# Kernel optimization log

Measured on AMD Instinct MI355X. Metric: run time of the kernel, lower is better.

Reference implementation:

```python
import jax, jax.numpy as jnp
import numpy as np

S = 1024   # query_len == key_len (self-attention)
B = 4      # batch
E = 1024   # embed_dim
H = 16     # num_heads
D = E // H # head_dim = 64
PE = 2 * S # positional table rows


def setup_inputs() -> dict:
    rng = jax.random.key(0)
    ks = jax.random.split(rng, 12)
    f = lambda k, sh, s: jax.random.normal(k, sh, dtype=jnp.float32) * s
    W = 0.02  # weight scale (xavier-ish for E=1024)
    return {
        'query': f(ks[0], (S, B, E), 1.0),
        'key': f(ks[1], (S, B, E), 1.0),
        'value': f(ks[2], (S, B, E), 1.0),
        'pe': f(ks[3], (PE, E), 1.0),
        'w_q': f(ks[4], (E, E), W),
        'w_k': f(ks[5], (E, E), W),
        'w_v': f(ks[6], (E, E), W),
        'w_k_pos': f(ks[7], (E, E), W),
        'content_bias': f(ks[8], (H, D), 0.02),
        'pos_bias': f(ks[9], (H, D), 0.02),
        'w_out': f(ks[10], (E, E), W),
        'b_out': f(ks[11], (E,), 0.02),
    }


def _rel_shift(pos):
    # pos: [B, H, Q, M] with M = 2*K - 1. Transformer-XL pad/narrow shift trick.
    Bn, h, Q, M = pos.shape
    p = jnp.pad(pos, ((0, 0), (0, 0), (0, 1), (0, 1)))          # [B,H,Q+1,M+1]
    p = p.reshape(Bn, h, (Q + 1) * (M + 1))
    p = p[:, :, M // 2: M // 2 + M * Q].reshape(Bn, h, Q, M)
    return p[..., :(M + 1) // 2]                                 # [B,H,Q,K]


def reference(query, key, value, pe, w_q, w_k, w_v, w_k_pos,
              content_bias, pos_bias, w_out, b_out):
    Q, Bn, Em = query.shape
    K = key.shape[0]
    h, d = content_bias.shape
    scaling = d ** -0.5

    # projections (nn.Linear: x @ W.T), split heads -> [B,H,len,d]
    q = (query @ w_q.T).reshape(Q, Bn, h, d).transpose(1, 2, 0, 3)
    k = (key   @ w_k.T).reshape(K, Bn, h, d).transpose(1, 2, 0, 3)
    v = (value @ w_v.T).reshape(K, Bn, h, d).transpose(1, 2, 0, 3)

    # relative position keys: centered slice of pe table, size 2K-1
    M = 2 * K - 1
    lower = pe.shape[0] // 2 - K + 1  # offset = 0
    k_pos = (pe[lower:lower + M] @ w_k_pos.T).reshape(M, h, d).transpose(1, 0, 2)  # [H,M,d]

    content = jnp.einsum('bhqd,bhkd->bhqk', q + content_bias[None, :, None, :], k)
    pos = jnp.einsum('bhqd,hmd->bhqm', q + pos_bias[None, :, None, :], k_pos)
    pos = _rel_shift(pos)  # [B,H,Q,K]

    attn = jax.nn.softmax((content + pos) * scaling, axis=-1)
    out = jnp.einsum('bhqk,bhkd->bhqd', attn, v)        # [B,H,Q,d]
    out = out.transpose(2, 0, 1, 3).reshape(Q, Bn, Em)  # [Q,B,E]
    return out @ w_out.T + b_out
```

## Files before the change

### kernel.cpp

```cpp
#include <hip/hip_runtime.h>


typedef short s16x8 __attribute__((ext_vector_type(8)));
typedef __bf16 bf16x8 __attribute__((ext_vector_type(8)));
typedef float f32x4 __attribute__((ext_vector_type(4)));
typedef unsigned int u32;

__device__ __forceinline__ float b2f(short s) {
  u32 u = ((u32)(unsigned short)s) << 16;
  return __builtin_bit_cast(float, u);
}
__device__ __forceinline__ short f2b(float f) {
  u32 u = __builtin_bit_cast(u32, f);
  u32 r = u + 0x7FFFu + ((u >> 16) & 1u);
  return (short)(r >> 16);
}

__device__ __forceinline__ f32x4 mfma_bf16(s16x8 a, s16x8 b, f32x4 c) {
  return __builtin_amdgcn_mfma_f32_16x16x32_bf16(
      __builtin_bit_cast(bf16x8, a), __builtin_bit_cast(bf16x8, b), c, 0, 0, 0);
}

__device__ __forceinline__ void glds16(void* l, const void* g) {
  __builtin_amdgcn_global_load_lds(
      (const __attribute__((address_space(1))) void*)g,
      (__attribute__((address_space(3))) void*)l, 16, 0, 0);
}

__device__ __forceinline__ int swz(int row, int unit) {
  return row * 128 + ((unit ^ (row & 7)) << 4);
}

__device__ __forceinline__ int pswz(int row, int col) {
  return (col & 7) | ((((col >> 3) ^ row) & 7) << 3);
}

__global__ __launch_bounds__(256) void cvt_all(
    const float* __restrict__ q, const float* __restrict__ k,
    const float* __restrict__ v, const float* __restrict__ pe,
    const float* __restrict__ wq, const float* __restrict__ wk,
    const float* __restrict__ wv, const float* __restrict__ wkp,
    const float* __restrict__ wo, short* __restrict__ dst)
{
  const int c = blockIdx.x * 256 + threadIdx.x;
  int idx = c * 8;
  const float* src;
  if      (idx < 4194304)  { src = q; }
  else if (idx < 8388608)  { src = k;   idx -= 4194304; }
  else if (idx < 12582912) { src = v;   idx -= 8388608; }
  else if (idx < 14680064) { src = pe;  idx -= 12582912; }
  else if (idx < 15728640) { src = wq;  idx -= 14680064; }
  else if (idx < 16777216) { src = wk;  idx -= 15728640; }
  else if (idx < 17825792) { src = wv;  idx -= 16777216; }
  else if (idx < 18874368) { src = wkp; idx -= 17825792; }
  else                     { src = wo;  idx -= 18874368; }
  float4 x = *(const float4*)(src + idx);
  float4 y = *(const float4*)(src + idx + 4);
  s16x8 o;
  o[0] = f2b(x.x); o[1] = f2b(x.y); o[2] = f2b(x.z); o[3] = f2b(x.w);
  o[4] = f2b(y.x); o[5] = f2b(y.y); o[6] = f2b(y.z); o[7] = f2b(y.w);
  *(s16x8*)(dst + (long)c * 8) = o;
}

__device__ __forceinline__ void gemm_core_bf16(
    const short* __restrict__ A, const short* __restrict__ W,
    short* At, short* Wt, f32x4 (&acc)[4][4], int bm, int bn)
{
  const int t = threadIdx.x;
  const int lane = t & 63, w = t >> 6;
  const int wm = w >> 1, wn = w & 1;
  const int quad = lane >> 4, lo16 = lane & 15;
  const int srow = t >> 2;
  const int skc = (t & 3) * 8;
  const int soff = t * 16;

  const short* Ag0 = A + (bm * 128 + srow) * 1024 + skc;
  const short* Wg0 = W + (bn * 128 + srow) * 1024 + skc;
  char* AtB = (char*)At;
  char* WtB = (char*)Wt;

  for (int k0 = 0; k0 < 1024; k0 += 32) {
    glds16(AtB + soff,        Ag0 + k0);
    glds16(AtB + 4096 + soff, Ag0 + 64 * 1024 + k0);
    glds16(WtB + soff,        Wg0 + k0);
    glds16(WtB + 4096 + soff, Wg0 + 64 * 1024 + k0);
    __syncthreads();
    s16x8 af[4], bfr[4];
#pragma unroll
    for (int mt = 0; mt < 4; ++mt)
      af[mt] = *(const s16x8*)(At + (wm * 64 + mt * 16 + lo16) * 32 + quad * 8);
#pragma unroll
    for (int nt = 0; nt < 4; ++nt)
      bfr[nt] = *(const s16x8*)(Wt + (wn * 64 + nt * 16 + lo16) * 32 + quad * 8);
#pragma unroll
    for (int mt = 0; mt < 4; ++mt)
#pragma unroll
      for (int nt = 0; nt < 4; ++nt)
        acc[mt][nt] = mfma_bf16(af[mt], bfr[nt], acc[mt][nt]);
    __syncthreads();
  }
}

__global__ __launch_bounds__(256) void proj_gemm(
    const short* __restrict__ qsrc, const short* __restrict__ ksrc,
    const short* __restrict__ vsrc, const short* __restrict__ pesrc,
    const short* __restrict__ wqb, const short* __restrict__ wkb,
    const short* __restrict__ wvb, const short* __restrict__ wkpb,
    short* __restrict__ qo, short* __restrict__ ko,
    short* __restrict__ vo, short* __restrict__ po)
{
  const int z = blockIdx.z;
  const short* A; const short* W; int M;
  if (z == 0)      { A = qsrc;  W = wqb;  M = 4096; }
  else if (z == 1) { A = ksrc;  W = wkb;  M = 4096; }
  else if (z == 2) { A = vsrc;  W = wvb;  M = 4096; }
  else             { A = pesrc; W = wkpb; M = 2048; }
  const int bm = blockIdx.x, bn = blockIdx.y;
  if (bm * 128 >= M) return;

  __shared__ __align__(16) short SH[8192];
  f32x4 acc[4][4] = {};
  gemm_core_bf16(A, W, SH, SH + 4096, acc, bm, bn);

  const int t = threadIdx.x;
  const int lane = t & 63, w = t >> 6;
  const int wm = w >> 1, wn = w & 1;
  const int quad = lane >> 4, lo16 = lane & 15;

  for (int hn = 0; hn < 2; ++hn) {
    __syncthreads();
    if (wn == hn) {
#pragma unroll
      for (int mt = 0; mt < 4; ++mt)
#pragma unroll
        for (int nt = 0; nt < 4; ++nt)
#pragma unroll
          for (int r = 0; r < 4; ++r) {
            const int row = wm * 64 + mt * 16 + quad * 4 + r;
            const int col = nt * 16 + lo16;
            SH[row * 64 + pswz(row, col)] = f2b(acc[mt][nt][r]);
          }
    }
    __syncthreads();
    const int hh = bn * 2 + hn;
    if (z <= 1) {
      short* o = (z == 0) ? qo : ko;
#pragma unroll
      for (int it = 0; it < 4; ++it) {
        const int item = t + 256 * it;
        const int ml = item >> 3;
        const int d0u = item & 7;
        s16x8 vls = *(const s16x8*)(SH + ml * 64 + ((d0u ^ (ml & 7)) << 3));
        const int m = bm * 128 + ml, s = m >> 2, b = m & 3;
        *(s16x8*)(o + (((b * 16 + hh) * 1024 + s) << 6) + d0u * 8) = vls;
      }
    } else if (z == 2) {
#pragma unroll
      for (int it = 0; it < 4; ++it) {
        const int item = t + 256 * it;
        const int d = item & 63;
        const int bb = (item >> 6) & 3;
        const int c = item >> 8;
        s16x8 vv;
#pragma unroll
        for (int i = 0; i < 8; ++i) {
          const int row = 32 * c + 4 * i + bb;
          vv[i] = SH[row * 64 + pswz(row, d)];
        }
        *(s16x8*)(vo + (((bb * 16 + hh) * 64 + d) << 10) + bm * 32 + 8 * c) = vv;
      }
    } else {
#pragma unroll
      for (int it = 0; it < 4; ++it) {
        const int item = t + 256 * it;
        const int ml = item >> 3;
        const int d0u = item & 7;
        s16x8 vls = *(const s16x8*)(SH + ml * 64 + ((d0u ^ (ml & 7)) << 3));
        const int m = bm * 128 + ml;
        *(s16x8*)(po + ((hh * 2048 + m) << 6) + d0u * 8) = vls;
      }
    }
  }
}

__global__ __launch_bounds__(256) void out_gemm(
    const short* __restrict__ A, const short* __restrict__ W,
    const float* __restrict__ bias, float* __restrict__ out)
{
  const int bm = blockIdx.x, bn = blockIdx.y;
  __shared__ __align__(16) short At[128 * 32];
  __shared__ __align__(16) short Wt[128 * 32];
  f32x4 acc[4][4] = {};
  gemm_core_bf16(A, W, At, Wt, acc, bm, bn);

  const int t = threadIdx.x;
  const int lane = t & 63, w = t >> 6;
  const int wm = w >> 1, wn = w & 1;
  const int quad = lane >> 4, lo16 = lane & 15;
#pragma unroll
  for (int mt = 0; mt < 4; ++mt) {
#pragma unroll
    for (int nt = 0; nt < 4; ++nt) {
#pragma unroll
      for (int r = 0; r < 4; ++r) {
        int m = bm * 128 + wm * 64 + mt * 16 + quad * 4 + r;
        int n = bn * 128 + wn * 64 + nt * 16 + lo16;
        out[m * 1024 + n] = acc[mt][nt][r] + bias[n];
      }
    }
  }
}

__device__ __forceinline__ void stage_attn(
    char* KtD, char* VtD, char* KPD,
    const char* gK, const char* gV, const char* gP,
    int k0, int q0, int t)
{
#pragma unroll
  for (int i = 0; i < 2; ++i) {
    const int o = t + 256 * i, row = o >> 3, u = (o & 7) ^ (row & 7);
    glds16(KtD + o * 16, gK + ((k0 + row) << 7) + (u << 4));
    glds16(VtD + o * 16, gV + (row << 11) + (k0 << 1) + (u << 4));
  }
#pragma unroll
  for (int i = 0; i < 4; ++i) {
    const int o = t + 256 * i, row = o >> 3, u = (o & 7) ^ (row & 7);
    int j = 961 + k0 - q0 + row;
    if (j > 2047) j = 2047;
    glds16(KPD + o * 16, gP + (j << 7) + (u << 4));
  }
}

__global__ __launch_bounds__(256) void attn_kernel(
    const short* __restrict__ qatt, const short* __restrict__ katt,
    const short* __restrict__ vT, const short* __restrict__ kpe,
    const float* __restrict__ cbias, const float* __restrict__ pbias,
    short* __restrict__ aout)
{
  const int q0 = blockIdx.x * 64;
  const int h = blockIdx.y;
  const int b = blockIdx.z;
  const int bh = b * 16 + h;
  const int t = threadIdx.x;
  const int w = t >> 6, lane = t & 63;
  const int quad = lane >> 4, lo16 = lane & 15;

  __shared__ __align__(16) char KtB[2][64 * 128];
  __shared__ __align__(16) char VtB[2][64 * 128];
  __shared__ __align__(16) char KPB[2][128 * 128];
  __shared__ __align__(16) char PtB[4][16 * 128];
  char* Pt_w = PtB[w];

  s16x8 a_c[2], a_p[2];
  {
    const int qg = q0 + 16 * w + lo16;
    const short* qrow = qatt + (bh * 1024 + qg) * 64;
#pragma unroll
    for (int ds = 0; ds < 2; ++ds) {
      const int d0 = ds * 32 + quad * 8;
      s16x8 qv = *(const s16x8*)(qrow + d0);
#pragma unroll
      for (int j = 0; j < 8; ++j) {
        float qf = b2f(qv[j]);
        a_c[ds][j] = f2b(qf + cbias[h * 64 + d0 + j]);
        a_p[ds][j] = f2b(qf + pbias[h * 64 + d0 + j]);
      }
    }
  }

  f32x4 O[4] = {};
  float lrow[4] = {0.f, 0.f, 0.f, 0.f};

  const int ro = 48 - 16 * w;

  const char* gK = (const char*)(katt + (size_t)bh * 65536);
  const char* gV = (const char*)(vT   + (size_t)bh * 65536);
  const char* gP = (const char*)(kpe  + (size_t)h * 131072);

  stage_attn(KtB[0], VtB[0], KPB[0], gK, gV, gP, 0,  q0, t);
  stage_attn(KtB[1], VtB[1], KPB[1], gK, gV, gP, 64, q0, t);

  int cur = 0;
  for (int kt = 0; kt < 16; ++kt) {
    asm volatile("s_waitcnt vmcnt(8)" ::: "memory");
    __builtin_amdgcn_sched_barrier(0);
    __builtin_amdgcn_s_barrier();
    __builtin_amdgcn_sched_barrier(0);

    const char* Kc  = KtB[cur];
    const char* Vc  = VtB[cur];
    const char* KPc = KPB[cur];

    float rot_cur[4];
    {
      f32x4 a = {0.f, 0.f, 0.f, 0.f};
      const int row = ro + lo16;
#pragma unroll
      for (int ds = 0; ds < 2; ++ds) {
        s16x8 bf = *(const s16x8*)(KPc + swz(row, ds * 4 + quad));
        a = mfma_bf16(a_p[ds], bf, a);
      }
#pragma unroll
      for (int r = 0; r < 4; ++r) {
        const int qi = quad * 4 + r;
        const int srclane = quad * 16 + ((lo16 + 15 - qi) & 15);
        rot_cur[r] = __shfl(a[r], srclane, 64);
      }
    }
#pragma unroll
    for (int nt = 0; nt < 4; ++nt) {
      f32x4 spn = {0.f, 0.f, 0.f, 0.f};
      {
        const int row = ro + (nt + 1) * 16 + lo16;
#pragma unroll
        for (int ds = 0; ds < 2; ++ds) {
          s16x8 bf = *(const s16x8*)(KPc + swz(row, ds * 4 + quad));
          spn = mfma_bf16(a_p[ds], bf, spn);
        }
      }
      f32x4 sc = {0.f, 0.f, 0.f, 0.f};
      {
        const int row = nt * 16 + lo16;
#pragma unroll
        for (int ds = 0; ds < 2; ++ds) {
          s16x8 bf = *(const s16x8*)(Kc + swz(row, ds * 4 + quad));
          sc = mfma_bf16(a_c[ds], bf, sc);
        }
      }
      const int col = nt * 16 + lo16;
#pragma unroll
      for (int rp = 0; rp < 2; ++rp) {
        float pv[2];
#pragma unroll
        for (int rr = 0; rr < 2; ++rr) {
          const int r = rp * 2 + rr;
          const int qi = quad * 4 + r;
          const int so = lo16 + 15 - qi;
          const int srclane = quad * 16 + (so & 15);
          const float rot_next = __shfl(spn[r], srclane, 64);
          const float pos = (so >= 16) ? rot_next : rot_cur[r];
          pv[rr] = __builtin_exp2f((sc[r] + pos) * 0.1803368801111244f);
          rot_cur[r] = rot_next;
        }
        u32 pk;
        asm("v_cvt_pk_bf16_f32 %0, %1, %2" : "=v"(pk) : "v"(pv[0]), "v"(pv[1]));
        lrow[rp * 2]     += __builtin_bit_cast(float, pk << 16);
        lrow[rp * 2 + 1] += __builtin_bit_cast(float, pk & 0xFFFF0000u);
        const int qi0 = quad * 4 + rp * 2, qi1 = qi0 + 1;
        *(short*)(Pt_w + qi0 * 128 + (((col >> 3) ^ (qi0 & 7)) << 4) +
                  ((col & 7) << 1)) = (short)pk;
        *(short*)(Pt_w + qi1 * 128 + (((col >> 3) ^ (qi1 & 7)) << 4) +
                  ((col & 7) << 1)) = (short)(pk >> 16);
      }
    }
    __builtin_amdgcn_wave_barrier();

    s16x8 ap[2];
#pragma unroll
    for (int ks = 0; ks < 2; ++ks)
      ap[ks] = *(const s16x8*)(Pt_w + swz(lo16, ks * 4 + quad));
    __builtin_amdgcn_wave_barrier();

#pragma unroll
    for (int ntd = 0; ntd < 4; ++ntd) {
#pragma unroll
      for (int ks = 0; ks < 2; ++ks) {
        s16x8 bv = *(const s16x8*)(Vc + swz(ntd * 16 + lo16, ks * 4 + quad));
        O[ntd] = mfma_bf16(ap[ks], bv, O[ntd]);
      }
    }

    __builtin_amdgcn_sched_barrier(0);
    __builtin_amdgcn_s_barrier();
    __builtin_amdgcn_sched_barrier(0);

    const int kn = (kt + 2 < 16) ? (kt + 2) * 64 : 960;
    stage_attn(KtB[cur], VtB[cur], KPB[cur], gK, gV, gP, kn, q0, t);
    cur ^= 1;
  }

#pragma unroll
  for (int r = 0; r < 4; ++r) {
#pragma unroll
    for (int off = 1; off < 16; off <<= 1)
      lrow[r] += __shfl_xor(lrow[r], off, 64);
    float rl = 1.f / lrow[r];
    int qg = q0 + 16 * w + quad * 4 + r;
#pragma unroll
    for (int ntd = 0; ntd < 4; ++ntd) {
      int d = ntd * 16 + lo16;
      aout[(qg * 4 + b) * 1024 + h * 64 + d] = f2b(O[ntd][r] * rl);
    }
  }
}

extern "C" void kernel_launch(void* const* d_in, const int* in_sizes, int n_in,
                              void* d_out, int out_size, void* d_ws, size_t ws_size,
                              hipStream_t stream) {
  (void)in_sizes; (void)n_in; (void)out_size; (void)ws_size;
  const float* query = (const float*)d_in[0];
  const float* key   = (const float*)d_in[1];
  const float* value = (const float*)d_in[2];
  const float* pe    = (const float*)d_in[3];
  const float* wq    = (const float*)d_in[4];
  const float* wk    = (const float*)d_in[5];
  const float* wv    = (const float*)d_in[6];
  const float* wkp   = (const float*)d_in[7];
  const float* cb    = (const float*)d_in[8];
  const float* pb    = (const float*)d_in[9];
  const float* wout  = (const float*)d_in[10];
  const float* bout  = (const float*)d_in[11];

  short* ws    = (short*)d_ws;
  short* qsrc  = ws;
  short* ksrc  = ws + 4194304;
  short* vsrc  = ws + 8388608;
  short* pesrc = ws + 12582912;
  short* wqb   = ws + 14680064;
  short* wkb   = ws + 15728640;
  short* wvb   = ws + 16777216;
  short* wkpb  = ws + 17825792;
  short* woutb = ws + 18874368;
  short* qatt  = ws + 19922944;
  short* katt  = ws + 24117248;
  short* vT    = ws + 28311552;
  short* kpe   = ws + 32505856;
  short* aout  = qsrc;

  cvt_all<<<dim3(9728), 256, 0, stream>>>(
      query, key, value, pe, wq, wk, wv, wkp, wout, ws);
  proj_gemm<<<dim3(32, 8, 4), 256, 0, stream>>>(
      qsrc, ksrc, vsrc, pesrc, wqb, wkb, wvb, wkpb, qatt, katt, vT, kpe);
  attn_kernel<<<dim3(16, 16, 4), 256, 0, stream>>>(
      qatt, katt, vT, kpe, cb, pb, aout);
  out_gemm<<<dim3(32, 8), 256, 0, stream>>>(aout, woutb, bout, (float*)d_out);
}
```

Before: 284.7 us.

## Double-buffer GEMM LDS tiles and use ring buffer for positional keys in attention

The projection and output GEMMs now use two LDS buffers with async global-to-LDS prefetch two steps ahead and raw s_barrier/waitcnt, replacing load-then-sync per K step. This lets global loads overlap the MFMA work. In attention, the overlapping 128-row positional-key window per tile is replaced by a 256-row circular buffer filled 64 new rows per iteration, so each KP row is loaded once instead of twice. The rotated carry (rot_cur) is kept across iterations instead of recomputed. This doubles GEMM LDS usage and adds modular indexing, and it depends on getting the waitcnt counts right.

```diff
diff --git a/kernel.cpp b/kernel.cpp
--- a/kernel.cpp
+++ b/kernel.cpp
@@ -62,9 +62,18 @@
   *(s16x8*)(dst + (long)c * 8) = o;
 }
 
-__device__ __forceinline__ void gemm_core_bf16(
+__device__ __forceinline__ void stage_gemm(char* AtD, char* WtD,
+    const short* Ag0, const short* Wg0, int k0, int soff)
+{
+  glds16(AtD + soff,        Ag0 + k0);
+  glds16(AtD + 4096 + soff, Ag0 + 65536 + k0);
+  glds16(WtD + soff,        Wg0 + k0);
+  glds16(WtD + 4096 + soff, Wg0 + 65536 + k0);
+}
+
+__device__ __forceinline__ void gemm_core_pipe(
     const short* __restrict__ A, const short* __restrict__ W,
-    short* At, short* Wt, f32x4 (&acc)[4][4], int bm, int bn)
+    short (*At)[4096], short (*Wt)[4096], f32x4 (&acc)[4][4], int bm, int bn)
 {
   const int t = threadIdx.x;
   const int lane = t & 63, w = t >> 6;
@@ -76,29 +85,38 @@
 
   const short* Ag0 = A + (bm * 128 + srow) * 1024 + skc;
   const short* Wg0 = W + (bn * 128 + srow) * 1024 + skc;
-  char* AtB = (char*)At;
-  char* WtB = (char*)Wt;
-
+
+  stage_gemm((char*)At[0], (char*)Wt[0], Ag0, Wg0, 0, soff);
+  stage_gemm((char*)At[1], (char*)Wt[1], Ag0, Wg0, 32, soff);
+
+  int cur = 0;
   for (int k0 = 0; k0 < 1024; k0 += 32) {
-    glds16(AtB + soff,        Ag0 + k0);
-    glds16(AtB + 4096 + soff, Ag0 + 64 * 1024 + k0);
-    glds16(WtB + soff,        Wg0 + k0);
-    glds16(WtB + 4096 + soff, Wg0 + 64 * 1024 + k0);
-    __syncthreads();
+    asm volatile("s_waitcnt vmcnt(4)" ::: "memory");
+    __builtin_amdgcn_sched_barrier(0);
+    __builtin_amdgcn_s_barrier();
+    __builtin_amdgcn_sched_barrier(0);
     s16x8 af[4], bfr[4];
 #pragma unroll
     for (int mt = 0; mt < 4; ++mt)
-      af[mt] = *(const s16x8*)(At + (wm * 64 + mt * 16 + lo16) * 32 + quad * 8);
+      af[mt] = *(const s16x8*)(At[cur] + (wm * 64 + mt * 16 + lo16) * 32 + quad * 8);
 #pragma unroll
     for (int nt = 0; nt < 4; ++nt)
-      bfr[nt] = *(const s16x8*)(Wt + (wn * 64 + nt * 16 + lo16) * 32 + quad * 8);
+      bfr[nt] = *(const s16x8*)(Wt[cur] + (wn * 64 + nt * 16 + lo16) * 32 + quad * 8);
 #pragma unroll
     for (int mt = 0; mt < 4; ++mt)
 #pragma unroll
       for (int nt = 0; nt < 4; ++nt)
         acc[mt][nt] = mfma_bf16(af[mt], bfr[nt], acc[mt][nt]);
-    __syncthreads();
-  }
+    __builtin_amdgcn_sched_barrier(0);
+    __builtin_amdgcn_s_barrier();
+    __builtin_amdgcn_sched_barrier(0);
+    const int kn = (k0 + 64 < 1024) ? (k0 + 64) : 992;
+    stage_gemm((char*)At[cur], (char*)Wt[cur], Ag0, Wg0, kn, soff);
+    cur ^= 1;
+  }
+  asm volatile("s_waitcnt vmcnt(0)" ::: "memory");
+  __builtin_amdgcn_sched_barrier(0);
+  __builtin_amdgcn_s_barrier();
 }
 
 __global__ __launch_bounds__(256) void proj_gemm(
@@ -118,9 +136,11 @@
   const int bm = blockIdx.x, bn = blockIdx.y;
   if (bm * 128 >= M) return;
 
-  __shared__ __align__(16) short SH[8192];
+  __shared__ __align__(16) short At[2][4096];
+  __shared__ __align__(16) short Wt[2][4096];
   f32x4 acc[4][4] = {};
-  gemm_core_bf16(A, W, SH, SH + 4096, acc, bm, bn);
+  gemm_core_pipe(A, W, At, Wt, acc, bm, bn);
+  short* SH = &At[0][0];
 
   const int t = threadIdx.x;
   const int lane = t & 63, w = t >> 6;
@@ -188,10 +208,10 @@
     const float* __restrict__ bias, float* __restrict__ out)
 {
   const int bm = blockIdx.x, bn = blockIdx.y;
-  __shared__ __align__(16) short At[128 * 32];
-  __shared__ __align__(16) short Wt[128 * 32];
+  __shared__ __align__(16) short At[2][4096];
+  __shared__ __align__(16) short Wt[2][4096];
   f32x4 acc[4][4] = {};
-  gemm_core_bf16(A, W, At, Wt, acc, bm, bn);
+  gemm_core_pipe(A, W, At, Wt, acc, bm, bn);
 
   const int t = threadIdx.x;
   const int lane = t & 63, w = t >> 6;
@@ -211,10 +231,8 @@
   }
 }
 
-__device__ __forceinline__ void stage_attn(
-    char* KtD, char* VtD, char* KPD,
-    const char* gK, const char* gV, const char* gP,
-    int k0, int q0, int t)
+__device__ __forceinline__ void stage_kv(char* KtD, char* VtD,
+    const char* gK, const char* gV, int k0, int t)
 {
 #pragma unroll
   for (int i = 0; i < 2; ++i) {
@@ -222,12 +240,19 @@
     glds16(KtD + o * 16, gK + ((k0 + row) << 7) + (u << 4));
     glds16(VtD + o * 16, gV + (row << 11) + (k0 << 1) + (u << 4));
   }
-#pragma unroll
-  for (int i = 0; i < 4; ++i) {
-    const int o = t + 256 * i, row = o >> 3, u = (o & 7) ^ (row & 7);
-    int j = 961 + k0 - q0 + row;
+}
+
+__device__ __forceinline__ void stage_kp64(char* KPR, const char* gP,
+    int rbase, int jbase, int t)
+{
+#pragma unroll
+  for (int i = 0; i < 2; ++i) {
+    const int o = t + 256 * i, row = o >> 3;
+    const int rr = rbase + row;
+    const int u = (o & 7) ^ (rr & 7);
+    int j = jbase + row;
     if (j > 2047) j = 2047;
-    glds16(KPD + o * 16, gP + (j << 7) + (u << 4));
+    glds16(KPR + rbase * 128 + o * 16, gP + (j << 7) + (u << 4));
   }
 }
 
@@ -247,7 +272,7 @@
 
   __shared__ __align__(16) char KtB[2][64 * 128];
   __shared__ __align__(16) char VtB[2][64 * 128];
-  __shared__ __align__(16) char KPB[2][128 * 128];
+  __shared__ __align__(16) char KPB[256 * 128];
   __shared__ __align__(16) char PtB[4][16 * 128];
   char* Pt_w = PtB[w];
 
@@ -272,32 +297,36 @@
   float lrow[4] = {0.f, 0.f, 0.f, 0.f};
 
   const int ro = 48 - 16 * w;
+  const int jb0 = 961 - q0;
 
   const char* gK = (const char*)(katt + (size_t)bh * 65536);
   const char* gV = (const char*)(vT   + (size_t)bh * 65536);
   const char* gP = (const char*)(kpe  + (size_t)h * 131072);
 
-  stage_attn(KtB[0], VtB[0], KPB[0], gK, gV, gP, 0,  q0, t);
-  stage_attn(KtB[1], VtB[1], KPB[1], gK, gV, gP, 64, q0, t);
-
+  stage_kv(KtB[0], VtB[0], gK, gV, 0, t);
+  stage_kp64(KPB, gP, 0,   jb0,       t);
+  stage_kp64(KPB, gP, 64,  jb0 + 64,  t);
+  stage_kv(KtB[1], VtB[1], gK, gV, 64, t);
+  stage_kp64(KPB, gP, 128, jb0 + 128, t);
+
+  float rot_cur[4];
   int cur = 0;
   for (int kt = 0; kt < 16; ++kt) {
-    asm volatile("s_waitcnt vmcnt(8)" ::: "memory");
+    asm volatile("s_waitcnt vmcnt(6)" ::: "memory");
     __builtin_amdgcn_sched_barrier(0);
     __builtin_amdgcn_s_barrier();
     __builtin_amdgcn_sched_barrier(0);
 
-    const char* Kc  = KtB[cur];
-    const char* Vc  = VtB[cur];
-    const char* KPc = KPB[cur];
-
-    float rot_cur[4];
-    {
+    const char* Kc = KtB[cur];
+    const char* Vc = VtB[cur];
+    const int rb = (64 * kt) & 255;
+
+    if (kt == 0) {
       f32x4 a = {0.f, 0.f, 0.f, 0.f};
-      const int row = ro + lo16;
+      const int rr = ro + lo16;
 #pragma unroll
       for (int ds = 0; ds < 2; ++ds) {
-        s16x8 bf = *(const s16x8*)(KPc + swz(row, ds * 4 + quad));
+        s16x8 bf = *(const s16x8*)(KPB + swz(rr, ds * 4 + quad));
         a = mfma_bf16(a_p[ds], bf, a);
       }
 #pragma unroll
@@ -307,14 +336,15 @@
         rot_cur[r] = __shfl(a[r], srclane, 64);
       }
     }
+
 #pragma unroll
     for (int nt = 0; nt < 4; ++nt) {
       f32x4 spn = {0.f, 0.f, 0.f, 0.f};
       {
-        const int row = ro + (nt + 1) * 16 + lo16;
+        const int rr = (rb + ro + (nt + 1) * 16 + lo16) & 255;
 #pragma unroll
         for (int ds = 0; ds < 2; ++ds) {
-          s16x8 bf = *(const s16x8*)(KPc + swz(row, ds * 4 + quad));
+          s16x8 bf = *(const s16x8*)(KPB + swz(rr, ds * 4 + quad));
           spn = mfma_bf16(a_p[ds], bf, spn);
         }
       }
@@ -332,14 +362,14 @@
       for (int rp = 0; rp < 2; ++rp) {
         float pv[2];
 #pragma unroll
-        for (int rr = 0; rr < 2; ++rr) {
-          const int r = rp * 2 + rr;
+        for (int rr2 = 0; rr2 < 2; ++rr2) {
+          const int r = rp * 2 + rr2;
           const int qi = quad * 4 + r;
           const int so = lo16 + 15 - qi;
           const int srclane = quad * 16 + (so & 15);
           const float rot_next = __shfl(spn[r], srclane, 64);
           const float pos = (so >= 16) ? rot_next : rot_cur[r];
-          pv[rr] = __builtin_exp2f((sc[r] + pos) * 0.1803368801111244f);
+          pv[rr2] = __builtin_exp2f((sc[r] + pos) * 0.1803368801111244f);
           rot_cur[r] = rot_next;
         }
         u32 pk;
@@ -375,7 +405,8 @@
     __builtin_amdgcn_sched_barrier(0);
 
     const int kn = (kt + 2 < 16) ? (kt + 2) * 64 : 960;
-    stage_attn(KtB[cur], VtB[cur], KPB[cur], gK, gV, gP, kn, q0, t);
+    stage_kv(KtB[cur], VtB[cur], gK, gV, kn, t);
+    stage_kp64(KPB, gP, (64 * kt + 192) & 255, jb0 + 64 * kt + 192, t);
     cur ^= 1;
   }
 
```

After: 277.4 us. 2.6% less time.
